# Optimization experiments

Measured on AMD Instinct MI355X. Metric: run time of the kernel, lower is better.

## Reference

```python
import jax, jax.numpy as jnp
import numpy as np

B = 8192
D_IN = 1024
D_H = 1024


def setup_inputs() -> dict:
    key = jax.random.key(0)
    ks = jax.random.split(key, 15)
    s_in = 1.0 / np.sqrt(D_IN)
    s_h = 1.0 / np.sqrt(D_H)
    return {
        "x": jax.random.normal(ks[0], (B, D_IN), dtype=jnp.float32),
        "h": jax.random.normal(ks[1], (B, D_H), dtype=jnp.float32),
        "c": jax.random.normal(ks[2], (B, D_H), dtype=jnp.float32),
        "Wi": jax.random.normal(ks[3], (D_H, D_IN), dtype=jnp.float32) * s_in,
        "bi": jax.random.normal(ks[4], (D_H,), dtype=jnp.float32) * s_in,
        "Ui": jax.random.normal(ks[5], (D_H, D_H), dtype=jnp.float32) * s_h,
        "Wf": jax.random.normal(ks[6], (D_H, D_IN), dtype=jnp.float32) * s_in,
        "bf": jax.random.normal(ks[7], (D_H,), dtype=jnp.float32) * s_in,
        "Uf": jax.random.normal(ks[8], (D_H, D_H), dtype=jnp.float32) * s_h,
        "Wo": jax.random.normal(ks[9], (D_H, D_IN), dtype=jnp.float32) * s_in,
        "bo": jax.random.normal(ks[10], (D_H,), dtype=jnp.float32) * s_in,
        "Uo": jax.random.normal(ks[11], (D_H, D_H), dtype=jnp.float32) * s_h,
        "Wc": jax.random.normal(ks[12], (D_H, D_IN), dtype=jnp.float32) * s_in,
        "bc": jax.random.normal(ks[13], (D_H,), dtype=jnp.float32) * s_in,
        "Uc": jax.random.normal(ks[14], (D_H, D_H), dtype=jnp.float32) * s_h,
    }


def reference(x, h, c, Wi, bi, Ui, Wf, bf, Uf, Wo, bo, Uo, Wc, bc, Uc):
    # torch Linear: y = x @ W.T + b, W is [out, in]. Same math as the 8
    # separate Linear calls, expressed as 2 concatenated GEMMs + fused gates.
    Wx = jnp.concatenate([Wi, Wf, Wo, Wc], axis=0)       # [4H, D_in]
    Uh = jnp.concatenate([Ui, Uf, Uo, Uc], axis=0)       # [4H, H]
    b = jnp.concatenate([bi, bf, bo, bc], axis=0)        # [4H]
    gates = x @ Wx.T + h @ Uh.T + b                       # [B, 4H]
    gi, gf, go, gc = jnp.split(gates, 4, axis=-1)
    i = jax.nn.sigmoid(gi)
    f = jax.nn.sigmoid(gf)
    o = jax.nn.sigmoid(go)
    c_ = jnp.tanh(gc)
    new_c = f * c + i * c_
    new_h = o * jnp.tanh(new_c)
    return new_h, new_c
```

## Files before the change

kernel.cpp:

```cpp
#include <hip/hip_runtime.h>
#include <stdint.h>

#define B_ROWS 8192
#define DH     1024
#define KTOT   2048

using short8 = __attribute__((ext_vector_type(8))) short;
using f32x4  = __attribute__((ext_vector_type(4))) float;

__device__ __forceinline__ short bfr(float f) {
    uint32_t u = __float_as_uint(f);
    u = (u + 0x7FFFu + ((u >> 16) & 1u)) >> 16;
    return (short)u;
}

__device__ __forceinline__ float sigm(float x) {
    x = fminf(fmaxf(x, -20.f), 20.f);
    return 1.f / (1.f + __expf(-x));
}
__device__ __forceinline__ float tanh_(float x) {
    x = fminf(fmaxf(x, -10.f), 10.f);
    float e = __expf(2.f * x);
    return (e - 1.f) / (e + 1.f);
}

__device__ __forceinline__ void gl16(const void* g, void* l) {
    __builtin_amdgcn_global_load_lds(
        (const __attribute__((address_space(1))) uint32_t*)(uintptr_t)g,
        (__attribute__((address_space(3))) uint32_t*)(uint32_t)(uintptr_t)l,
        16, 0, 0);
}

__global__ __launch_bounds__(256) void build_A(const float* __restrict__ x,
                                               const float* __restrict__ h,
                                               short* __restrict__ A) {
    int t   = blockIdx.x * 256 + threadIdx.x;
    int row = t >> 8;
    int col = (t & 255) * 8;
    const float* src = (col < 1024) ? (x + (size_t)row * 1024 + col)
                                    : (h + (size_t)row * 1024 + (col - 1024));
    float4 f0 = ((const float4*)src)[0];
    float4 f1 = ((const float4*)src)[1];
    short8 o;
    o[0] = bfr(f0.x); o[1] = bfr(f0.y); o[2] = bfr(f0.z); o[3] = bfr(f0.w);
    o[4] = bfr(f1.x); o[5] = bfr(f1.y); o[6] = bfr(f1.z); o[7] = bfr(f1.w);
    *(short8*)(A + (size_t)row * KTOT + col) = o;
}

__global__ __launch_bounds__(256) void build_W(
        const float* __restrict__ Wi, const float* __restrict__ Ui,
        const float* __restrict__ Wf, const float* __restrict__ Uf,
        const float* __restrict__ Wo, const float* __restrict__ Uo,
        const float* __restrict__ Wc, const float* __restrict__ Uc,
        short* __restrict__ Wcat) {
    int row  = blockIdx.x;
    int col  = threadIdx.x * 8;
    int gate = row >> 10;
    int n    = row & 1023;
    const float* Wg = (gate == 0) ? Wi : (gate == 1) ? Wf : (gate == 2) ? Wo : Wc;
    const float* Ug = (gate == 0) ? Ui : (gate == 1) ? Uf : (gate == 2) ? Uo : Uc;
    const float* src = (col < 1024) ? (Wg + (size_t)n * 1024 + col)
                                    : (Ug + (size_t)n * 1024 + (col - 1024));
    float4 f0 = ((const float4*)src)[0];
    float4 f1 = ((const float4*)src)[1];
    short8 o;
    o[0] = bfr(f0.x); o[1] = bfr(f0.y); o[2] = bfr(f0.z); o[3] = bfr(f0.w);
    o[4] = bfr(f1.x); o[5] = bfr(f1.y); o[6] = bfr(f1.z); o[7] = bfr(f1.w);
    *(short8*)(Wcat + (size_t)row * KTOT + col) = o;
}

__global__ __launch_bounds__(256, 2) void lstm_main(
        const short* __restrict__ A, const short* __restrict__ Wcat,
        const float* __restrict__ bi, const float* __restrict__ bff,
        const float* __restrict__ bo, const float* __restrict__ bc,
        const float* __restrict__ cin, float* __restrict__ out) {
    __shared__ __align__(16) short At[128 * 32];
    __shared__ __align__(16) short Bt[128 * 32];

    const int tid  = threadIdx.x;
    const int lane = tid & 63;
    const int wave = tid >> 6;
    const int wr   = wave >> 1, wc = wave & 1;
    const int l15  = lane & 15, l16 = lane >> 4;
    const int col0 = blockIdx.x * 128;
    const int row0 = blockIdx.y * 128;

    const int srow = tid >> 2;
    const int scg  = (tid & 3) * 8;
    const short* gA0 = A + (size_t)(row0 + srow) * KTOT + scg;
    const short* gA1 = gA0 + (size_t)64 * KTOT;
    short* lA0 = At + tid * 8;
    short* lA1 = At + tid * 8 + 2048;
    short* lB0 = Bt + tid * 8;
    short* lB1 = Bt + tid * 8 + 2048;

    const int aoff = (wr * 64 + l15) * 32 + l16 * 8;
    const int boff = (wc * 64 + l15) * 32 + l16 * 8;

    f32x4 acc[4][4];
    float st[4][4][4];
    #pragma unroll
    for (int mi = 0; mi < 4; ++mi)
        #pragma unroll
        for (int ni = 0; ni < 4; ++ni)
            acc[mi][ni] = f32x4{0.f, 0.f, 0.f, 0.f};

    const int   gateof[4] = {0, 3, 1, 2};
    const float* biasp[4] = {bi, bc, bff, bo};

    #pragma unroll
    for (int pass = 0; pass < 4; ++pass) {
        const short* pb0 = Wcat + (size_t)(gateof[pass] * 1024 + col0 + srow) * KTOT + scg;
        const short* pb1 = pb0 + (size_t)64 * KTOT;
        const short* pa0 = gA0;
        const short* pa1 = gA1;

        for (int kt = 0; kt < KTOT / 32; ++kt) {
            gl16(pa0, lA0); gl16(pa1, lA1);
            gl16(pb0, lB0); gl16(pb1, lB1);
            pa0 += 32; pa1 += 32; pb0 += 32; pb1 += 32;
            __syncthreads();
            short8 af[4], bf8[4];
            #pragma unroll
            for (int mi = 0; mi < 4; ++mi)
                af[mi] = *(const short8*)(At + aoff + mi * 16 * 32);
            #pragma unroll
            for (int ni = 0; ni < 4; ++ni)
                bf8[ni] = *(const short8*)(Bt + boff + ni * 16 * 32);
            #pragma unroll
            for (int mi = 0; mi < 4; ++mi)
                #pragma unroll
                for (int ni = 0; ni < 4; ++ni)
                    acc[mi][ni] = __builtin_amdgcn_mfma_f32_16x16x32_bf16(
                        af[mi], bf8[ni], acc[mi][ni], 0, 0, 0);
            __syncthreads();
        }

        const float* bp = biasp[pass];
        #pragma unroll
        for (int ni = 0; ni < 4; ++ni) {
            const int col = col0 + wc * 64 + ni * 16 + l15;
            const float bv = bp[col];
            #pragma unroll
            for (int mi = 0; mi < 4; ++mi) {
                const int rbase = row0 + wr * 64 + mi * 16 + l16 * 4;
                #pragma unroll
                for (int r = 0; r < 4; ++r) {
                    float g = acc[mi][ni][r] + bv;
                    if (pass == 0) {
                        st[mi][ni][r] = sigm(g);
                    } else if (pass == 1) {
                        st[mi][ni][r] *= tanh_(g);
                    } else if (pass == 2) {
                        const size_t row = (size_t)(rbase + r);
                        float cv = cin[row * DH + col];
                        float nc = sigm(g) * cv + st[mi][ni][r];
                        out[(size_t)B_ROWS * DH + row * DH + col] = nc;
                        st[mi][ni][r] = tanh_(nc);
                    } else {
                        const size_t row = (size_t)(rbase + r);
                        out[row * DH + col] = sigm(g) * st[mi][ni][r];
                    }
                    acc[mi][ni][r] = 0.f;
                }
            }
        }
    }
}

extern "C" void kernel_launch(void* const* d_in, const int* in_sizes, int n_in,
                              void* d_out, int out_size, void* d_ws, size_t ws_size,
                              hipStream_t stream) {
    (void)in_sizes; (void)n_in; (void)out_size; (void)ws_size;
    const float* x  = (const float*)d_in[0];
    const float* h  = (const float*)d_in[1];
    const float* c  = (const float*)d_in[2];
    const float* Wi = (const float*)d_in[3];
    const float* bi = (const float*)d_in[4];
    const float* Ui = (const float*)d_in[5];
    const float* Wf = (const float*)d_in[6];
    const float* bf = (const float*)d_in[7];
    const float* Uf = (const float*)d_in[8];
    const float* Wo = (const float*)d_in[9];
    const float* bo = (const float*)d_in[10];
    const float* Uo = (const float*)d_in[11];
    const float* Wc = (const float*)d_in[12];
    const float* bc = (const float*)d_in[13];
    const float* Uc = (const float*)d_in[14];
    float* out = (float*)d_out;

    short* A    = (short*)d_ws;
    short* Wcat = A + (size_t)B_ROWS * KTOT;

    hipLaunchKernelGGL(build_A, dim3(8192), dim3(256), 0, stream, x, h, A);
    hipLaunchKernelGGL(build_W, dim3(4096), dim3(256), 0, stream,
                       Wi, Ui, Wf, Uf, Wo, Uo, Wc, Uc, Wcat);
    hipLaunchKernelGGL(lstm_main, dim3(8, 64), dim3(256), 0, stream,
                       A, Wcat, bi, bf, bo, bc, c, out);
}
```

Baseline: 447.8 us.

## Interleave gate weight rows so each MFMA tile holds all four gates

The weight matrix is rebuilt with the four gate rows of each hidden unit interleaved, and the GEMM is transposed so weights form the M dimension. Each accumulator's four register lanes then carry i, f, o, c for one element, so the epilogue fuses all gates in registers. This removes the four sequential K passes per block and the cross-pass state. The grid becomes a flat 2048-block launch with a swizzled tile order for L2 reuse, and launch bounds are raised to 4 blocks per CU. The epilogue now writes outputs strided across columns, which is less coalesced.

New measurement: 385.7 us. 1.16x faster.

```diff
diff --git a/kernel.cpp b/kernel.cpp
--- a/kernel.cpp
+++ b/kernel.cpp
@@ -4,6 +4,7 @@
 #define B_ROWS 8192
 #define DH     1024
 #define KTOT   2048
+#define GC     4096
 
 using short8 = __attribute__((ext_vector_type(8))) short;
 using f32x4  = __attribute__((ext_vector_type(4))) float;
@@ -52,11 +53,11 @@
         const float* __restrict__ Wf, const float* __restrict__ Uf,
         const float* __restrict__ Wo, const float* __restrict__ Uo,
         const float* __restrict__ Wc, const float* __restrict__ Uc,
-        short* __restrict__ Wcat) {
+        short* __restrict__ Wrow) {
     int row  = blockIdx.x;
     int col  = threadIdx.x * 8;
-    int gate = row >> 10;
-    int n    = row & 1023;
+    int n    = row >> 2;
+    int gate = row & 3;
     const float* Wg = (gate == 0) ? Wi : (gate == 1) ? Wf : (gate == 2) ? Wo : Wc;
     const float* Ug = (gate == 0) ? Ui : (gate == 1) ? Uf : (gate == 2) ? Uo : Uc;
     const float* src = (col < 1024) ? (Wg + (size_t)n * 1024 + col)
@@ -66,15 +67,15 @@
     short8 o;
     o[0] = bfr(f0.x); o[1] = bfr(f0.y); o[2] = bfr(f0.z); o[3] = bfr(f0.w);
     o[4] = bfr(f1.x); o[5] = bfr(f1.y); o[6] = bfr(f1.z); o[7] = bfr(f1.w);
-    *(short8*)(Wcat + (size_t)row * KTOT + col) = o;
+    *(short8*)(Wrow + (size_t)row * KTOT + col) = o;
 }
 
-__global__ __launch_bounds__(256, 2) void lstm_main(
-        const short* __restrict__ A, const short* __restrict__ Wcat,
+__global__ __launch_bounds__(256, 4) void lstm_main(
+        const short* __restrict__ A, const short* __restrict__ Wrow,
         const float* __restrict__ bi, const float* __restrict__ bff,
         const float* __restrict__ bo, const float* __restrict__ bc,
         const float* __restrict__ cin, float* __restrict__ out) {
-    __shared__ __align__(16) short At[128 * 32];
+    __shared__ __align__(16) short Wt[128 * 32];
     __shared__ __align__(16) short Bt[128 * 32];
 
     const int tid  = threadIdx.x;
@@ -82,15 +83,23 @@
     const int wave = tid >> 6;
     const int wr   = wave >> 1, wc = wave & 1;
     const int l15  = lane & 15, l16 = lane >> 4;
-    const int col0 = blockIdx.x * 128;
-    const int row0 = blockIdx.y * 128;
+
+    const int nwg = gridDim.x;
+    const int bid = blockIdx.x;
+    const int swz = (bid & 7) * (nwg >> 3) + (bid >> 3);
+    const int mtile = swz & 31;
+    const int ntile = swz >> 5;
+    const int m0 = mtile * 128;
+    const int n0 = ntile * 128;
 
     const int srow = tid >> 2;
     const int scg  = (tid & 3) * 8;
-    const short* gA0 = A + (size_t)(row0 + srow) * KTOT + scg;
-    const short* gA1 = gA0 + (size_t)64 * KTOT;
-    short* lA0 = At + tid * 8;
-    short* lA1 = At + tid * 8 + 2048;
+    const short* pw0 = Wrow + (size_t)(m0 + srow) * KTOT + scg;
+    const short* pw1 = pw0 + (size_t)64 * KTOT;
+    const short* pa0 = A + (size_t)(n0 + srow) * KTOT + scg;
+    const short* pa1 = pa0 + (size_t)64 * KTOT;
+    short* lW0 = Wt + tid * 8;
+    short* lW1 = Wt + tid * 8 + 2048;
     short* lB0 = Bt + tid * 8;
     short* lB1 = Bt + tid * 8 + 2048;
 
@@ -98,72 +107,53 @@
     const int boff = (wc * 64 + l15) * 32 + l16 * 8;
 
     f32x4 acc[4][4];
-    float st[4][4][4];
     #pragma unroll
     for (int mi = 0; mi < 4; ++mi)
         #pragma unroll
         for (int ni = 0; ni < 4; ++ni)
             acc[mi][ni] = f32x4{0.f, 0.f, 0.f, 0.f};
 
-    const int   gateof[4] = {0, 3, 1, 2};
-    const float* biasp[4] = {bi, bc, bff, bo};
-
-    #pragma unroll
-    for (int pass = 0; pass < 4; ++pass) {
-        const short* pb0 = Wcat + (size_t)(gateof[pass] * 1024 + col0 + srow) * KTOT + scg;
-        const short* pb1 = pb0 + (size_t)64 * KTOT;
-        const short* pa0 = gA0;
-        const short* pa1 = gA1;
-
-        for (int kt = 0; kt < KTOT / 32; ++kt) {
-            gl16(pa0, lA0); gl16(pa1, lA1);
-            gl16(pb0, lB0); gl16(pb1, lB1);
-            pa0 += 32; pa1 += 32; pb0 += 32; pb1 += 32;
-            __syncthreads();
-            short8 af[4], bf8[4];
-            #pragma unroll
-            for (int mi = 0; mi < 4; ++mi)
-                af[mi] = *(const short8*)(At + aoff + mi * 16 * 32);
+    for (int kt = 0; kt < KTOT / 32; ++kt) {
+        gl16(pw0, lW0); gl16(pw1, lW1);
+        gl16(pa0, lB0); gl16(pa1, lB1);
+        pw0 += 32; pw1 += 32; pa0 += 32; pa1 += 32;
+        __syncthreads();
+        short8 wf[4], af[4];
+        #pragma unroll
+        for (int mi = 0; mi < 4; ++mi)
+            wf[mi] = *(const short8*)(Wt + aoff + mi * 16 * 32);
+        #pragma unroll
+        for (int ni = 0; ni < 4; ++ni)
+            af[ni] = *(const short8*)(Bt + boff + ni * 16 * 32);
+        #pragma unroll
+        for (int mi = 0; mi < 4; ++mi)
             #pragma unroll
             for (int ni = 0; ni < 4; ++ni)
-                bf8[ni] = *(const short8*)(Bt + boff + ni * 16 * 32);
-            #pragma unroll
-            for (int mi = 0; mi < 4; ++mi)
-                #pragma unroll
-                for (int ni = 0; ni < 4; ++ni)
-                    acc[mi][ni] = __builtin_amdgcn_mfma_f32_16x16x32_bf16(
-                        af[mi], bf8[ni], acc[mi][ni], 0, 0, 0);
-            __syncthreads();
-        }
+                acc[mi][ni] = __builtin_amdgcn_mfma_f32_16x16x32_bf16(
+                    wf[mi], af[ni], acc[mi][ni], 0, 0, 0);
+        __syncthreads();
+    }
 
-        const float* bp = biasp[pass];
+    const int hbase = (m0 >> 2) + wr * 16;
+    #pragma unroll
+    for (int mi = 0; mi < 4; ++mi) {
+        const int hcol = hbase + mi * 4 + l16;
+        const float bvi = bi[hcol];
+        const float bvf = bff[hcol];
+        const float bvo = bo[hcol];
+        const float bvc = bc[hcol];
         #pragma unroll
         for (int ni = 0; ni < 4; ++ni) {
-            const int col = col0 + wc * 64 + ni * 16 + l15;
-            const float bv = bp[col];
-            #pragma unroll
-            for (int mi = 0; mi < 4; ++mi) {
-                const int rbase = row0 + wr * 64 + mi * 16 + l16 * 4;
-                #pragma unroll
-                for (int r = 0; r < 4; ++r) {
-                    float g = acc[mi][ni][r] + bv;
-                    if (pass == 0) {
-                        st[mi][ni][r] = sigm(g);
-                    } else if (pass == 1) {
-                        st[mi][ni][r] *= tanh_(g);
-                    } else if (pass == 2) {
-                        const size_t row = (size_t)(rbase + r);
-                        float cv = cin[row * DH + col];
-                        float nc = sigm(g) * cv + st[mi][ni][r];
-                        out[(size_t)B_ROWS * DH + row * DH + col] = nc;
-                        st[mi][ni][r] = tanh_(nc);
-                    } else {
-                        const size_t row = (size_t)(rbase + r);
-                        out[row * DH + col] = sigm(g) * st[mi][ni][r];
-                    }
-                    acc[mi][ni][r] = 0.f;
-                }
-            }
+            const size_t brow = (size_t)(n0 + wc * 64 + ni * 16 + l15);
+            const float cv = cin[brow * DH + hcol];
+            const float gi = acc[mi][ni][0] + bvi;
+            const float gf = acc[mi][ni][1] + bvf;
+            const float go = acc[mi][ni][2] + bvo;
+            const float gc = acc[mi][ni][3] + bvc;
+            const float nc = sigm(gf) * cv + sigm(gi) * tanh_(gc);
+            const float nh = sigm(go) * tanh_(nc);
+            out[brow * DH + hcol] = nh;
+            out[(size_t)B_ROWS * DH + brow * DH + hcol] = nc;
         }
     }
 }
@@ -190,11 +180,11 @@
     float* out = (float*)d_out;
 
     short* A    = (short*)d_ws;
-    short* Wcat = A + (size_t)B_ROWS * KTOT;
+    short* Wrow = A + (size_t)B_ROWS * KTOT;
 
     hipLaunchKernelGGL(build_A, dim3(8192), dim3(256), 0, stream, x, h, A);
     hipLaunchKernelGGL(build_W, dim3(4096), dim3(256), 0, stream,
-                       Wi, Ui, Wf, Uf, Wo, Uo, Wc, Uc, Wcat);
-    hipLaunchKernelGGL(lstm_main, dim3(8, 64), dim3(256), 0, stream,
-                       A, Wcat, bi, bf, bo, bc, c, out);
+                       Wi, Ui, Wf, Uf, Wo, Uo, Wc, Uc, Wrow);
+    hipLaunchKernelGGL(lstm_main, dim3(2048), dim3(256), 0, stream,
+                       A, Wrow, bi, bf, bo, bc, c, out);
 }
```
